# Kernel optimization log

Hardware: AMD Instinct MI355X
Metric: run time of the kernel (lower is better)

## Reference

```python
import jax, jax.numpy as jnp
import numpy as np


def setup_inputs() -> dict:
    key = jax.random.key(0)
    k1, k2, k3, k4 = jax.random.split(key, 4)
    B, Cin, Cout, N, modes = 16, 128, 128, 8192, 64
    scale = 1.0 / (Cin * Cout)
    x = jax.random.normal(k1, (B, Cin, N), dtype=jnp.float32)
    # spectral weight: [in, out, modes, 2] uniform in [0, scale) like torch.rand * scale
    w_spec = scale * jax.random.uniform(k2, (Cin, Cout, modes, 2), dtype=jnp.float32)
    # Conv1d(kernel=1) weight [out, in] and bias [out] (kaiming-uniform-ish init)
    bound = 1.0 / np.sqrt(Cin)
    w_conv = jax.random.uniform(k3, (Cout, Cin), minval=-bound, maxval=bound, dtype=jnp.float32)
    b_conv = jax.random.uniform(k4, (Cout,), minval=-bound, maxval=bound, dtype=jnp.float32)
    return {"x": x, "w_spec": w_spec, "w_conv": w_conv, "b_conv": b_conv}


def reference(x, w_spec, w_conv, b_conv):
    N = x.shape[-1]
    modes = w_spec.shape[2]
    n_freq = N // 2 + 1
    # Spectral conv: rfft, keep first `modes` coefficients, complex channel mix
    x_ft = jnp.fft.rfft(x)  # [B, Cin, n_freq] complex64
    w_c = w_spec[..., 0] + 1j * w_spec[..., 1]  # [Cin, Cout, modes]
    out_m = jnp.einsum('bim,iom->bom', x_ft[:, :, :modes], w_c)  # [B, Cout, modes]
    out_ft = jnp.pad(out_m, ((0, 0), (0, 0), (0, n_freq - modes)))
    x1 = jnp.fft.irfft(out_ft, n=N)  # [B, Cout, N]
    # 1x1 conv (pointwise channel mix)
    x2 = jnp.einsum('bin,oi->bon', x, w_conv) + b_conv[None, :, None]
    return jax.nn.gelu(x1 + x2, approximate=False)
```

## Files before the change

kernel.cpp:

```cpp
#include <hip/hip_runtime.h>
#include <hip/hip_bf16.h>
#include <math.h>

#define NB    16
#define NCIN  128
#define NCOUT 128
#define NN    8192
#define NMOD  64

typedef short bf16x8 __attribute__((ext_vector_type(8)));
typedef float f32x4  __attribute__((ext_vector_type(4)));

#define MFMA16(a, b, c) __builtin_amdgcn_mfma_f32_16x16x32_bf16((a), (b), (c), 0, 0, 0)

__device__ inline unsigned short f2bf_rne(float f) {
    unsigned u = __float_as_uint(f);
    u += 0x7FFF + ((u >> 16) & 1);
    return (unsigned short)(u >> 16);
}
__device__ inline short f2bf_trunc(float f) {
    return (short)(__float_as_uint(f) >> 16);
}

__global__ __launch_bounds__(256) void k_prep(const float* __restrict__ wc,
                                              const float* __restrict__ wsp,
                                              unsigned short* __restrict__ T,
                                              unsigned short* __restrict__ Tt,
                                              unsigned short* __restrict__ Wcb,
                                              unsigned short* __restrict__ Wpk) {
    const float C = 7.66990393943e-4f;
    if (blockIdx.x < 16) {
        int a = blockIdx.x * 256 + threadIdx.x;
        int k = a >> 6, n0 = (a & 63) * 128;
        for (int j8 = 0; j8 < 16; ++j8) {
            short c8[8], s8[8];
            #pragma unroll
            for (int j = 0; j < 8; ++j) {
                int n = n0 + j8 * 8 + j;
                int ph = (k * n) & (NN - 1);
                float sn, cs; __sincosf((float)ph * C, &sn, &cs);
                c8[j] = (short)f2bf_rne(cs);
                s8[j] = (short)f2bf_rne(-sn);
            }
            *(bf16x8*)(T + (size_t)(2 * k) * NN + n0 + j8 * 8)     = *(bf16x8*)c8;
            *(bf16x8*)(T + (size_t)(2 * k + 1) * NN + n0 + j8 * 8) = *(bf16x8*)s8;
        }
    } else if (blockIdx.x < 48) {
        int n = (blockIdx.x - 16) * 256 + threadIdx.x;
        for (int k4 = 0; k4 < 16; ++k4) {
            short buf[8];
            #pragma unroll
            for (int j = 0; j < 4; ++j) {
                int k = k4 * 4 + j;
                int ph = (n * k) & (NN - 1);
                float sn, cs; __sincosf((float)ph * C, &sn, &cs);
                buf[2 * j]     = (short)f2bf_rne(cs);
                buf[2 * j + 1] = (short)f2bf_rne(-sn);
            }
            *(bf16x8*)(Tt + (size_t)n * 128 + k4 * 8) = *(bf16x8*)buf;
        }
    } else if (blockIdx.x < 112) {
        int j = (blockIdx.x - 48) * 256 + threadIdx.x;
        if (j < NCOUT * NCIN) Wcb[j] = f2bf_rne(wc[j]);
    } else {
        int g2 = (blockIdx.x - 112) * 256 + threadIdx.x;
        int k  = g2 & 63;
        int o  = (g2 >> 6) & 127;
        int ch = g2 >> 13;
        const float s = (k == 0) ? (1.f / NN) : (2.f / NN);
        const float2* wp = (const float2*)wsp;
        unsigned short* wre = Wpk + ((size_t)(k * 2 + 0) * 128 + o) * 256;
        unsigned short* wim = Wpk + ((size_t)(k * 2 + 1) * 128 + o) * 256;
        for (int c = ch * 8; c < ch * 8 + 8; ++c) {
            int i0 = 4 * c;
            short re8[8], im8[8];
            #pragma unroll
            for (int t2 = 0; t2 < 4; ++t2) {
                float2 wv = wp[((size_t)(i0 + t2) * 128 + o) * 64 + k];
                float wr = s * wv.x, wi = s * wv.y;
                re8[2 * t2]     = (short)f2bf_rne(wr);
                re8[2 * t2 + 1] = (short)f2bf_rne(-wi);
                im8[2 * t2]     = (k == 0) ? (short)0 : (short)f2bf_rne(wi);
                im8[2 * t2 + 1] = (k == 0) ? (short)0 : (short)f2bf_rne(wr);
            }
            *(bf16x8*)(wre + c * 8) = *(bf16x8*)re8;
            *(bf16x8*)(wim + c * 8) = *(bf16x8*)im8;
        }
    }
}

__global__ __launch_bounds__(256) void k_dftmm(const float* __restrict__ x,
                                               const unsigned short* __restrict__ T,
                                               float* __restrict__ Cpart) {
    const int mt = blockIdx.x & 31, sp = blockIdx.x >> 5;
    const int w = threadIdx.x >> 6, l = threadIdx.x & 63;
    const int l15 = l & 15, q = l >> 4;
    const int colbase = w * 32;
    f32x4 acc[4][2] = {};
    for (int kt = 0; kt < 16; ++kt) {
        const int kb = sp * 512 + kt * 32;
        bf16x8 a[4], bb[2];
        #pragma unroll
        for (int mf = 0; mf < 4; ++mf) {
            const float* ap = x + (size_t)(mt * 64 + mf * 16 + l15) * NN + kb + q * 8;
            float4 f0 = *(const float4*)ap;
            float4 f1 = *(const float4*)(ap + 4);
            short t8[8] = { f2bf_trunc(f0.x), f2bf_trunc(f0.y), f2bf_trunc(f0.z), f2bf_trunc(f0.w),
                            f2bf_trunc(f1.x), f2bf_trunc(f1.y), f2bf_trunc(f1.z), f2bf_trunc(f1.w) };
            a[mf] = *(bf16x8*)t8;
        }
        #pragma unroll
        for (int nf = 0; nf < 2; ++nf)
            bb[nf] = *(const bf16x8*)(T + (size_t)(colbase + nf * 16 + l15) * NN + kb + q * 8);
        #pragma unroll
        for (int mf = 0; mf < 4; ++mf) {
            acc[mf][0] = MFMA16(a[mf], bb[0], acc[mf][0]);
            acc[mf][1] = MFMA16(a[mf], bb[1], acc[mf][1]);
        }
    }
    #pragma unroll
    for (int mf = 0; mf < 4; ++mf)
        #pragma unroll
        for (int nf = 0; nf < 2; ++nf) {
            int col  = colbase + nf * 16 + l15;
            int row0 = mt * 64 + mf * 16 + q * 4;
            *(f32x4*)(Cpart + (size_t)sp * 262144 + (size_t)col * 2048 + row0) = acc[mf][nf];
        }
}

__global__ __launch_bounds__(256) void k_reduce(const float* __restrict__ Cpart,
                                                float* __restrict__ Xf) {
    int t = blockIdx.x * 256 + threadIdx.x;
    float s = 0.f;
    #pragma unroll
    for (int sp = 0; sp < 16; ++sp) s += Cpart[(size_t)sp * 262144 + t];
    Xf[t] = s;
}

__global__ __launch_bounds__(64) void k_mixmm(const float* __restrict__ Xf,
                                              const unsigned short* __restrict__ Wpk,
                                              unsigned short* __restrict__ Aspec) {
    const int k = blockIdx.x >> 2, oq = blockIdx.x & 3;
    const int l = threadIdx.x, l15 = l & 15, q = l >> 4;
    f32x4 ar[2] = {}, ai[2] = {};
    const float* xr = Xf + (size_t)(2 * k) * 2048 + l15 * 128;
    const float* xi = xr + 2048;
    #pragma unroll
    for (int kt = 0; kt < 8; ++kt) {
        int i0 = kt * 16 + q * 4;
        float4 r4 = *(const float4*)(xr + i0);
        float4 i4 = *(const float4*)(xi + i0);
        short a8[8] = { (short)f2bf_rne(r4.x), (short)f2bf_rne(i4.x),
                        (short)f2bf_rne(r4.y), (short)f2bf_rne(i4.y),
                        (short)f2bf_rne(r4.z), (short)f2bf_rne(i4.z),
                        (short)f2bf_rne(r4.w), (short)f2bf_rne(i4.w) };
        bf16x8 a = *(bf16x8*)a8;
        #pragma unroll
        for (int nf = 0; nf < 2; ++nf) {
            int o = oq * 32 + nf * 16 + l15;
            const unsigned short* wb = Wpk + ((size_t)(k * 2) * 128 + o) * 256 + kt * 32 + q * 8;
            bf16x8 bre = *(const bf16x8*)wb;
            bf16x8 bim = *(const bf16x8*)(wb + 32768);
            ar[nf] = MFMA16(a, bre, ar[nf]);
            ai[nf] = MFMA16(a, bim, ai[nf]);
        }
    }
    #pragma unroll
    for (int nf = 0; nf < 2; ++nf) {
        int o = oq * 32 + nf * 16 + l15;
        #pragma unroll
        for (int r = 0; r < 4; ++r) {
            int b = q * 4 + r;
            unsigned v = (unsigned)f2bf_rne(ar[nf][r]) | ((unsigned)f2bf_rne(ai[nf][r]) << 16);
            *(unsigned*)(Aspec + ((size_t)b * 128 + o) * 128 + 2 * k) = v;
        }
    }
}

__global__ __launch_bounds__(256) void k_out(const float* __restrict__ x,
                                             const unsigned short* __restrict__ Tt,
                                             const unsigned short* __restrict__ Aspec,
                                             const unsigned short* __restrict__ Wcb,
                                             const float* __restrict__ bias,
                                             float* __restrict__ out) {
    const int b = blockIdx.x >> 6, nt = blockIdx.x & 63;
    const int w = threadIdx.x >> 6, l = threadIdx.x & 63;
    const int l15 = l & 15, q = l >> 4;
    __shared__ short xs[16384];

    const float* xb = x + (size_t)b * 128 * NN + nt * 128;
    #pragma unroll
    for (int it = 0; it < 8; ++it) {
        int unit = it * 256 + threadIdx.x;
        int ipair = unit >> 5, nq = unit & 31;
        int i0 = ipair * 2;
        const float* p0 = xb + (size_t)i0 * NN + nq * 4;
        float4 r0 = *(const float4*)p0;
        float4 r1 = *(const float4*)(p0 + NN);
        float a0[4] = { r0.x, r0.y, r0.z, r0.w };
        float a1[4] = { r1.x, r1.y, r1.z, r1.w };
        #pragma unroll
        for (int j = 0; j < 4; ++j) {
            int n = nq * 4 + j;
            unsigned v = (unsigned)(unsigned short)f2bf_trunc(a0[j])
                       | ((unsigned)(unsigned short)f2bf_trunc(a1[j]) << 16);
            int addr = n * 128 + (((i0 >> 3) ^ (n & 15)) * 8) + (i0 & 7);
            *(unsigned*)&xs[addr] = v;
        }
    }

    f32x4 acc[8][2] = {};
    #pragma unroll
    for (int kt = 0; kt < 4; ++kt) {
        bf16x8 bb[2];
        #pragma unroll
        for (int nf = 0; nf < 2; ++nf) {
            int n = nt * 128 + w * 32 + nf * 16 + l15;
            bb[nf] = *(const bf16x8*)(Tt + (size_t)n * 128 + kt * 32 + q * 8);
        }
        const unsigned short* Ap = Aspec + (size_t)b * 16384 + kt * 32 + q * 8;
        #pragma unroll
        for (int mf = 0; mf < 8; ++mf) {
            bf16x8 a = *(const bf16x8*)(Ap + (size_t)(mf * 16 + l15) * 128);
            acc[mf][0] = MFMA16(a, bb[0], acc[mf][0]);
            acc[mf][1] = MFMA16(a, bb[1], acc[mf][1]);
        }
    }
    __syncthreads();
    #pragma unroll
    for (int kt = 0; kt < 4; ++kt) {
        bf16x8 bb[2];
        #pragma unroll
        for (int nf = 0; nf < 2; ++nf) {
            int nl = w * 32 + nf * 16 + l15;
            int c  = kt * 4 + q;
            bb[nf] = *(const bf16x8*)&xs[nl * 128 + ((c ^ (nl & 15)) * 8)];
        }
        const unsigned short* Ap = Wcb + kt * 32 + q * 8;
        #pragma unroll
        for (int mf = 0; mf < 8; ++mf) {
            bf16x8 a = *(const bf16x8*)(Ap + (size_t)(mf * 16 + l15) * 128);
            acc[mf][0] = MFMA16(a, bb[0], acc[mf][0]);
            acc[mf][1] = MFMA16(a, bb[1], acc[mf][1]);
        }
    }
    #pragma unroll
    for (int mf = 0; mf < 8; ++mf)
        #pragma unroll
        for (int nf = 0; nf < 2; ++nf)
            #pragma unroll
            for (int r = 0; r < 4; ++r) {
                int o = mf * 16 + q * 4 + r;
                int n = nt * 128 + w * 32 + nf * 16 + l15;
                float v = acc[mf][nf][r] + bias[o];
                float u = v * v;
                float p = v * fmaf(0.0713548162f, u, 1.5957691216f);
                float e = __expf(-p);
                float g = v * __builtin_amdgcn_rcpf(1.f + e);
                out[((size_t)(b * 128 + o)) * NN + n] = g;
            }
}

extern "C" void kernel_launch(void* const* d_in, const int* in_sizes, int n_in,
                              void* d_out, int out_size, void* d_ws, size_t ws_size,
                              hipStream_t stream) {
    const float* x    = (const float*)d_in[0];
    const float* wsp  = (const float*)d_in[1];
    const float* wc   = (const float*)d_in[2];
    const float* bc   = (const float*)d_in[3];
    float* out = (float*)d_out;

    unsigned short* T   = (unsigned short*)d_ws;
    unsigned short* Tt  = T + (size_t)1048576;
    unsigned short* Wcb = Tt + (size_t)1048576;
    unsigned short* Asp = Wcb + 16384;
    unsigned short* Wpk = Asp + 262144;
    float* Cpart = (float*)(Wpk + (size_t)8388608);
    float* Xf    = Cpart + (size_t)16 * 262144;

    k_prep  <<<240,  256, 0, stream>>>(wc, wsp, T, Tt, Wcb, Wpk);
    k_dftmm <<<512,  256, 0, stream>>>(x, T, Cpart);
    k_reduce<<<1024, 256, 0, stream>>>(Cpart, Xf);
    k_mixmm <<<256,  64,  0, stream>>>(Xf, Wpk, Asp);
    k_out   <<<1024, 256, 0, stream>>>(x, Tt, Asp, Wcb, bc, out);
}
```

Measured before the change: 221.3 us.

## Pre-convert x to bf16 in a separate pass, reuse it in DFT and output GEMMs

Adds a conversion kernel that reads fp32 x once and writes a bf16 copy in [b][n][i] layout, plus an optional [b][i][n] copy when the workspace is large enough. The DFT GEMM and the output kernel then read bf16 directly, so the output kernel no longer needs its LDS staging and transpose. The reduce kernel is vectorized to float4. This trades an extra full pass over x and extra workspace traffic for halved reads in the later kernels, and the workspace-size check decides whether the bf16 path is used in the DFT GEMM.

```diff
diff --git a/kernel.cpp b/kernel.cpp
--- a/kernel.cpp
+++ b/kernel.cpp
@@ -9,6 +9,7 @@
 #define NMOD  64
 
 typedef short bf16x8 __attribute__((ext_vector_type(8)));
+typedef short bf16x4 __attribute__((ext_vector_type(4)));
 typedef float f32x4  __attribute__((ext_vector_type(4)));
 
 #define MFMA16(a, b, c) __builtin_amdgcn_mfma_f32_16x16x32_bf16((a), (b), (c), 0, 0, 0)
@@ -20,6 +21,36 @@
 }
 __device__ inline short f2bf_trunc(float f) {
     return (short)(__float_as_uint(f) >> 16);
+}
+
+__global__ __launch_bounds__(256) void k_cvt(const float* __restrict__ x,
+                                             unsigned short* __restrict__ xbn,
+                                             unsigned short* __restrict__ xbt,
+                                             int write_xbn) {
+    const int b = blockIdx.x >> 8, nt = blockIdx.x & 255;
+    const int i4 = (threadIdx.x & 31) * 4, ng = threadIdx.x >> 5;
+    const int n0 = nt * 32 + ng * 4;
+    const float* xp = x + ((size_t)b * 128 + i4) * NN + n0;
+    float rr[4][4];
+    #pragma unroll
+    for (int j = 0; j < 4; ++j) {
+        float4 r = *(const float4*)(xp + (size_t)j * NN);
+        rr[j][0] = r.x; rr[j][1] = r.y; rr[j][2] = r.z; rr[j][3] = r.w;
+    }
+    #pragma unroll
+    for (int c = 0; c < 4; ++c) {
+        short v[4] = { f2bf_trunc(rr[0][c]), f2bf_trunc(rr[1][c]),
+                       f2bf_trunc(rr[2][c]), f2bf_trunc(rr[3][c]) };
+        *(bf16x4*)(xbt + ((size_t)b * NN + n0 + c) * 128 + i4) = *(bf16x4*)v;
+    }
+    if (write_xbn) {
+        #pragma unroll
+        for (int j = 0; j < 4; ++j) {
+            short v[4] = { f2bf_trunc(rr[j][0]), f2bf_trunc(rr[j][1]),
+                           f2bf_trunc(rr[j][2]), f2bf_trunc(rr[j][3]) };
+            *(bf16x4*)(xbn + ((size_t)b * 128 + i4 + j) * NN + n0) = *(bf16x4*)v;
+        }
+    }
 }
 
 __global__ __launch_bounds__(256) void k_prep(const float* __restrict__ wc,
@@ -89,7 +120,9 @@
     }
 }
 
+template<bool BF16SRC>
 __global__ __launch_bounds__(256) void k_dftmm(const float* __restrict__ x,
+                                               const unsigned short* __restrict__ xbn,
                                                const unsigned short* __restrict__ T,
                                                float* __restrict__ Cpart) {
     const int mt = blockIdx.x & 31, sp = blockIdx.x >> 5;
@@ -102,12 +135,17 @@
         bf16x8 a[4], bb[2];
         #pragma unroll
         for (int mf = 0; mf < 4; ++mf) {
-            const float* ap = x + (size_t)(mt * 64 + mf * 16 + l15) * NN + kb + q * 8;
-            float4 f0 = *(const float4*)ap;
-            float4 f1 = *(const float4*)(ap + 4);
-            short t8[8] = { f2bf_trunc(f0.x), f2bf_trunc(f0.y), f2bf_trunc(f0.z), f2bf_trunc(f0.w),
-                            f2bf_trunc(f1.x), f2bf_trunc(f1.y), f2bf_trunc(f1.z), f2bf_trunc(f1.w) };
-            a[mf] = *(bf16x8*)t8;
+            const size_t roff = (size_t)(mt * 64 + mf * 16 + l15) * NN + kb + q * 8;
+            if (BF16SRC) {
+                a[mf] = *(const bf16x8*)(xbn + roff);
+            } else {
+                const float* ap = x + roff;
+                float4 f0 = *(const float4*)ap;
+                float4 f1 = *(const float4*)(ap + 4);
+                short t8[8] = { f2bf_trunc(f0.x), f2bf_trunc(f0.y), f2bf_trunc(f0.z), f2bf_trunc(f0.w),
+                                f2bf_trunc(f1.x), f2bf_trunc(f1.y), f2bf_trunc(f1.z), f2bf_trunc(f1.w) };
+                a[mf] = *(bf16x8*)t8;
+            }
         }
         #pragma unroll
         for (int nf = 0; nf < 2; ++nf)
@@ -131,10 +169,11 @@
 __global__ __launch_bounds__(256) void k_reduce(const float* __restrict__ Cpart,
                                                 float* __restrict__ Xf) {
     int t = blockIdx.x * 256 + threadIdx.x;
-    float s = 0.f;
-    #pragma unroll
-    for (int sp = 0; sp < 16; ++sp) s += Cpart[(size_t)sp * 262144 + t];
-    Xf[t] = s;
+    f32x4 s = {};
+    #pragma unroll
+    for (int sp = 0; sp < 16; ++sp)
+        s += *(const f32x4*)(Cpart + (size_t)sp * 262144 + (size_t)t * 4);
+    *(f32x4*)(Xf + (size_t)t * 4) = s;
 }
 
 __global__ __launch_bounds__(64) void k_mixmm(const float* __restrict__ Xf,
@@ -177,7 +216,7 @@
     }
 }
 
-__global__ __launch_bounds__(256) void k_out(const float* __restrict__ x,
+__global__ __launch_bounds__(256) void k_out(const unsigned short* __restrict__ xbt,
                                              const unsigned short* __restrict__ Tt,
                                              const unsigned short* __restrict__ Aspec,
                                              const unsigned short* __restrict__ Wcb,
@@ -186,36 +225,14 @@
     const int b = blockIdx.x >> 6, nt = blockIdx.x & 63;
     const int w = threadIdx.x >> 6, l = threadIdx.x & 63;
     const int l15 = l & 15, q = l >> 4;
-    __shared__ short xs[16384];
-
-    const float* xb = x + (size_t)b * 128 * NN + nt * 128;
-    #pragma unroll
-    for (int it = 0; it < 8; ++it) {
-        int unit = it * 256 + threadIdx.x;
-        int ipair = unit >> 5, nq = unit & 31;
-        int i0 = ipair * 2;
-        const float* p0 = xb + (size_t)i0 * NN + nq * 4;
-        float4 r0 = *(const float4*)p0;
-        float4 r1 = *(const float4*)(p0 + NN);
-        float a0[4] = { r0.x, r0.y, r0.z, r0.w };
-        float a1[4] = { r1.x, r1.y, r1.z, r1.w };
-        #pragma unroll
-        for (int j = 0; j < 4; ++j) {
-            int n = nq * 4 + j;
-            unsigned v = (unsigned)(unsigned short)f2bf_trunc(a0[j])
-                       | ((unsigned)(unsigned short)f2bf_trunc(a1[j]) << 16);
-            int addr = n * 128 + (((i0 >> 3) ^ (n & 15)) * 8) + (i0 & 7);
-            *(unsigned*)&xs[addr] = v;
-        }
-    }
-
+    const int nbase = nt * 128 + w * 32;
     f32x4 acc[8][2] = {};
     #pragma unroll
     for (int kt = 0; kt < 4; ++kt) {
         bf16x8 bb[2];
         #pragma unroll
         for (int nf = 0; nf < 2; ++nf) {
-            int n = nt * 128 + w * 32 + nf * 16 + l15;
+            int n = nbase + nf * 16 + l15;
             bb[nf] = *(const bf16x8*)(Tt + (size_t)n * 128 + kt * 32 + q * 8);
         }
         const unsigned short* Ap = Aspec + (size_t)b * 16384 + kt * 32 + q * 8;
@@ -226,15 +243,13 @@
             acc[mf][1] = MFMA16(a, bb[1], acc[mf][1]);
         }
     }
-    __syncthreads();
     #pragma unroll
     for (int kt = 0; kt < 4; ++kt) {
         bf16x8 bb[2];
         #pragma unroll
         for (int nf = 0; nf < 2; ++nf) {
-            int nl = w * 32 + nf * 16 + l15;
-            int c  = kt * 4 + q;
-            bb[nf] = *(const bf16x8*)&xs[nl * 128 + ((c ^ (nl & 15)) * 8)];
+            int n = nbase + nf * 16 + l15;
+            bb[nf] = *(const bf16x8*)(xbt + ((size_t)b * NN + n) * 128 + kt * 32 + q * 8);
         }
         const unsigned short* Ap = Wcb + kt * 32 + q * 8;
         #pragma unroll
@@ -251,7 +266,7 @@
             #pragma unroll
             for (int r = 0; r < 4; ++r) {
                 int o = mf * 16 + q * 4 + r;
-                int n = nt * 128 + w * 32 + nf * 16 + l15;
+                int n = nbase + nf * 16 + l15;
                 float v = acc[mf][nf][r] + bias[o];
                 float u = v * v;
                 float p = v * fmaf(0.0713548162f, u, 1.5957691216f);
@@ -275,12 +290,19 @@
     unsigned short* Wcb = Tt + (size_t)1048576;
     unsigned short* Asp = Wcb + 16384;
     unsigned short* Wpk = Asp + 262144;
-    float* Cpart = (float*)(Wpk + (size_t)8388608);
+    unsigned short* Xbt = Wpk + (size_t)8388608;
+    float* Cpart = (float*)(Xbt + (size_t)16777216);
     float* Xf    = Cpart + (size_t)16 * 262144;
-
+    unsigned short* Xbn = (unsigned short*)(Xf + 262144);
+    const int use_xbn = (ws_size >= (size_t)107000000) ? 1 : 0;
+
+    k_cvt   <<<4096, 256, 0, stream>>>(x, Xbn, Xbt, use_xbn);
     k_prep  <<<240,  256, 0, stream>>>(wc, wsp, T, Tt, Wcb, Wpk);
-    k_dftmm <<<512,  256, 0, stream>>>(x, T, Cpart);
-    k_reduce<<<1024, 256, 0, stream>>>(Cpart, Xf);
+    if (use_xbn)
+        k_dftmm<true> <<<512, 256, 0, stream>>>(x, Xbn, T, Cpart);
+    else
+        k_dftmm<false><<<512, 256, 0, stream>>>(x, Xbn, T, Cpart);
+    k_reduce<<<256,  256, 0, stream>>>(Cpart, Xf);
     k_mixmm <<<256,  64,  0, stream>>>(Xf, Wpk, Asp);
-    k_out   <<<1024, 256, 0, stream>>>(x, Tt, Asp, Wcb, bc, out);
-}
+    k_out   <<<1024, 256, 0, stream>>>(Xbt, Tt, Asp, Wcb, bc, out);
+}
```

New measurement: 257.2 us. 1.16x slower.
